# Optimization experiments

Hardware: AMD Instinct MI355X
Metric: run time of the kernel (lower is better)

## Reference

```python
import jax, jax.numpy as jnp
import numpy as np

V, NEIGH, C, N, H = 20000, 12, 16, 8, 4


def _circulant_basis(n):
    eye = jnp.eye(n, dtype=jnp.float32)
    return jnp.stack([jnp.roll(eye, b, axis=1) for b in range(n)])  # [n, n, n]


def setup_inputs() -> dict:
    key = jax.random.key(0)
    ks = jax.random.split(key, 12)
    x = jax.random.normal(ks[0], (V, C, N), dtype=jnp.float32)
    neighbors = jax.random.randint(ks[1], (V, NEIGH), 0, V)
    mask = jax.random.bernoulli(ks[2], 0.8, (V, NEIGH))
    pt = jax.random.normal(ks[3], (V, NEIGH, N, N), dtype=jnp.float32)
    rel_pos_u = jax.random.normal(ks[4], (V, NEIGH, 2), dtype=jnp.float32) * 0.1
    reg_basis = _circulant_basis(N)                                   # [N, N, N]
    value_basis1 = jax.random.normal(ks[5], (N, 2, N, N), dtype=jnp.float32)
    value_basis2 = jax.random.normal(ks[6], (N, 3, N, N), dtype=jnp.float32)
    s = 1.0 / np.sqrt(C * N)
    query_coeffs = jax.random.normal(ks[7], (H, C, N), dtype=jnp.float32) * s
    key_coeffs = jax.random.normal(ks[8], (H, C, N), dtype=jnp.float32) * s
    value0_params = jax.random.normal(ks[9], (H, C, N), dtype=jnp.float32) * s
    value1_params = jax.random.normal(ks[10], (H, C, N), dtype=jnp.float32) * s
    value2_params = jax.random.normal(ks[11], (H, C, N), dtype=jnp.float32) * s
    wm_weights = jax.random.normal(jax.random.fold_in(key, 99), (C, H * C, N), dtype=jnp.float32) * np.sqrt(2.0 / (H * C * N))
    return {"x": x, "neighbors": neighbors, "mask": mask,
            "parallel_transport_matrices": pt, "rel_pos_u": rel_pos_u,
            "reg_basis": reg_basis, "value_basis1": value_basis1,
            "value_basis2": value_basis2, "query_coeffs": query_coeffs,
            "key_coeffs": key_coeffs, "value0_params": value0_params,
            "value1_params": value1_params, "value2_params": value2_params,
            "wm_weights": wm_weights}


def reference(x, neighbors, mask, parallel_transport_matrices, rel_pos_u,
              reg_basis, value_basis1, value_basis2, query_coeffs, key_coeffs,
              value0_params, value1_params, value2_params, wm_weights):
    Nv, Cc, Nn = x.shape
    Hh = query_coeffs.shape[0]
    m = mask.astype(x.dtype)                                   # [v, n]
    x_neigh = x[neighbors] * m[:, :, None, None]               # [v, n, c, N]
    f = jnp.einsum('vnij,vncj->vnci', parallel_transport_matrices, x_neigh)
    # attention scores
    WQ = jnp.einsum('hcb,bij->hcij', query_coeffs, reg_basis)
    Q = jnp.einsum('hcij,vcj->vhi', WQ, x)                     # [v, h, N]
    WK = jnp.einsum('hcb,bij->hcij', key_coeffs, reg_basis)
    K = jnp.einsum('hcij,vncj->vnhi', WK, f)                   # [v, n, h, N]
    score = jax.nn.relu(Q[:, None] + K).mean(-1)               # [v, n, h]
    score = jnp.where(mask[:, :, None], score, 0.0)
    den = score.sum(axis=1)                                    # [v, h]
    dead = den < 1e-6
    n_valid = jnp.clip(m.sum(axis=1, keepdims=True), 1.0)      # [v, 1]
    uniform = m[:, :, None] / n_valid[:, :, None]              # [v, n, 1]
    attn = jnp.where(dead[:, None, :], uniform,
                     score / jnp.clip(den, 1e-6)[:, None, :])  # [v, n, h]
    # Taylor-basis values
    u0, u1 = rel_pos_u[..., 0], rel_pos_u[..., 1]
    u_quad = jnp.stack([u0 * u0, 2.0 * u0 * u1, u1 * u1], axis=-1)  # [v, n, 3]
    W0 = jnp.einsum('hcb,bij->hcij', value0_params, reg_basis)
    values = jnp.einsum('hcij,vncj->vnhci', W0, f)
    W1 = jnp.einsum('hcb,boij->hcoij', value1_params, value_basis1)
    values = values + jnp.einsum('hcoij,vncj,vno->vnhci', W1, f, rel_pos_u)
    W2 = jnp.einsum('hcb,boij->hcoij', value2_params, value_basis2)
    values = values + jnp.einsum('hcoij,vncj,vno->vnhci', W2, f, u_quad)
    head = jnp.einsum('vnh,vnhci->vhci', attn, values)         # [v, h, c, N]
    head = head.reshape(Nv, Hh * Cc, Nn)
    WM = jnp.einsum('ocb,bij->ocij', wm_weights, reg_basis)
    return jnp.einsum('ocij,vcj->voi', WM, head)               # [v, c, N]
```

## Files before the change

### kernel.cpp

```cpp
#include <hip/hip_runtime.h>

#define NV  20000
#define NNB 12
#define NC  16
#define NH  4
#define VC  4
#define GRID (NV/VC)

#define OFF_QC   0
#define OFF_KC   528
#define OFF_Q    1056
#define OFF_F    1184
#define OFF_HEAD 1184
#define OFF_SC   7520
#define OFF_DEN  7712
#define OFF_NV   7728
#define OFF_S4   7736
#define OFF_S2   7928
#define OFF_NB   8024
#define OFF_M    8072
#define SMEM_FL  8120

#define LD8(dst, off) { const float4 _a = *(const float4*)&smem[(off)]; \
                        const float4 _b = *(const float4*)&smem[(off)+4]; \
                        dst[0]=_a.x; dst[1]=_a.y; dst[2]=_a.z; dst[3]=_a.w; \
                        dst[4]=_b.x; dst[5]=_b.y; dst[6]=_b.z; dst[7]=_b.w; }
#define ST8(off, src) { *(float4*)&smem[(off)]   = make_float4(src[0],src[1],src[2],src[3]); \
                        *(float4*)&smem[(off)+4] = make_float4(src[4],src[5],src[6],src[7]); }

__global__ __launch_bounds__(256) void kprep(
    const float* __restrict__ v0p, const float* __restrict__ v1p,
    const float* __restrict__ v2p, const float* __restrict__ vb1,
    const float* __restrict__ vb2, float* __restrict__ A4,
    const unsigned char* __restrict__ m, int* __restrict__ flag)
{
    const int b = blockIdx.x, tid = threadIdx.x;
    if (b < 96) {
        int idx = b * 256 + tid;
        int j = idx & 7;
        int t = idx >> 3;
        int hc = t & 63; t >>= 6;
        int i = t & 7;
        int p = t >> 3;
        int h = hc >> 4, c = hc & 15;
        float s = 0.f;
        if (p == 0) {
            s = v0p[h*128 + c*8 + ((j - i + 8) & 7)];
        } else if (p <= 2) {
            int o = p - 1;
            #pragma unroll
            for (int bb = 0; bb < 8; ++bb)
                s += v1p[h*128 + c*8 + bb] * vb1[((bb*2 + o)*8 + i)*8 + j];
        } else {
            int o = p - 3;
            #pragma unroll
            for (int bb = 0; bb < 8; ++bb)
                s += v2p[h*128 + c*8 + bb] * vb2[((bb*3 + o)*8 + i)*8 + j];
        }
        A4[idx] = s;
    } else {
        __shared__ int s_nz;
        if (tid == 0) s_nz = 0;
        __syncthreads();
        int nz = 0;
        for (int k = (b - 96) * 256 + tid; k < NV * NNB; k += 64 * 256) {
            if ((k & 3) != 0 && m[k] != 0) nz = 1;
        }
        if (nz) atomicOr(&s_nz, 1);
        __syncthreads();
        if (tid == 0 && s_nz) atomicOr(flag, 1);
    }
}

__global__ __launch_bounds__(256, 4) void kmain(
    const float* __restrict__ x, const int* __restrict__ nbr,
    const unsigned char* __restrict__ mskb, const float* __restrict__ pt,
    const float* __restrict__ rel, const float* __restrict__ qc,
    const float* __restrict__ kc, const float* __restrict__ A4,
    const float* __restrict__ wm, const int* __restrict__ flagp,
    float* __restrict__ out)
{
    const int tid = threadIdx.x;
    const int vbase = blockIdx.x * VC;
    const int bytemode = flagp[0];
    const int* mski = (const int*)mskb;

    __shared__ __align__(16) float smem[SMEM_FL];

    for (int k = tid; k < 512; k += 256) {
        smem[OFF_QC + (k>>7)*132 + (k&127)] = qc[k];
        smem[OFF_KC + (k>>7)*132 + (k&127)] = kc[k];
    }
    if (tid < VC*NNB) {
        int gi = vbase*NNB + tid;
        ((int*)smem)[OFF_NB + tid] = nbr[gi];
        int raw = bytemode ? (int)mskb[gi] : mski[gi];
        smem[OFF_M + tid] = raw ? 1.0f : 0.0f;
    }
    if (tid >= 64 && tid < 64 + VC*NNB) {
        int vn = tid - 64;
        float u0 = rel[(vbase*NNB + vn)*2 + 0];
        float u1 = rel[(vbase*NNB + vn)*2 + 1];
        smem[OFF_S4+vn*4+0] = 1.0f;
        smem[OFF_S4+vn*4+1] = u0;
        smem[OFF_S4+vn*4+2] = u1;
        smem[OFF_S4+vn*4+3] = u0*u0;
        smem[OFF_S2+vn*2+0] = 2.0f*u0*u1;
        smem[OFF_S2+vn*2+1] = u1*u1;
    }
    __syncthreads();

    if (tid < 192) {
        const int vn = tid >> 2, cq = tid & 3;
        const int nb = ((const int*)smem)[OFF_NB + vn];
        const float m = smem[OFF_M + vn];
        const float4* xg = (const float4*)(x + (size_t)nb*128 + cq*32);
        float xnf[32];
        #pragma unroll
        for (int q = 0; q < 8; ++q) {
            float4 tv = xg[q];
            xnf[q*4+0]=tv.x; xnf[q*4+1]=tv.y; xnf[q*4+2]=tv.z; xnf[q*4+3]=tv.w;
        }
        const float* ptg = pt + (size_t)(vbase*NNB + vn)*64;
        float acc[4][8];
        #pragma unroll
        for (int c4 = 0; c4 < 4; ++c4)
            #pragma unroll
            for (int i = 0; i < 8; ++i) acc[c4][i] = 0.f;
        #pragma unroll
        for (int i = 0; i < 8; ++i) {
            const float4 pA = *(const float4*)(ptg + i*8);
            const float4 pB = *(const float4*)(ptg + i*8 + 4);
            float pj[8] = {pA.x,pA.y,pA.z,pA.w,pB.x,pB.y,pB.z,pB.w};
            #pragma unroll
            for (int c4 = 0; c4 < 4; ++c4)
                #pragma unroll
                for (int j = 0; j < 8; ++j)
                    acc[c4][i] += pj[j] * xnf[c4*8 + j];
        }
        #pragma unroll
        for (int c4 = 0; c4 < 4; ++c4) {
            int c = cq*4 + c4;
            float w[8];
            #pragma unroll
            for (int i = 0; i < 8; ++i) w[i] = m * acc[c4][i];
            ST8(OFF_F + vn*132 + c*8, w);
        }
    }
    __syncthreads();

    float K8[8] = {0,0,0,0,0,0,0,0};
    if (tid < 128) {
        const int cs = tid & 7, vh = tid >> 3, v = vh >> 2, h = vh & 3;
        const float* xrow = x + (size_t)(vbase + v)*128;
        float Q8[8] = {0,0,0,0,0,0,0,0};
        #pragma unroll
        for (int t = 0; t < 2; ++t) {
            int c = cs*2 + t;
            const float4 xa = *(const float4*)(xrow + c*8);
            const float4 xb = *(const float4*)(xrow + c*8 + 4);
            float xv[8] = {xa.x,xa.y,xa.z,xa.w,xb.x,xb.y,xb.z,xb.w};
            float qv[8]; LD8(qv, OFF_QC + h*132 + c*8);
            #pragma unroll
            for (int s = 0; s < 8; ++s)
                #pragma unroll
                for (int i = 0; i < 8; ++i)
                    Q8[i] += qv[s] * xv[(i+s)&7];
        }
        #pragma unroll
        for (int msk = 1; msk < 8; msk <<= 1)
            #pragma unroll
            for (int i = 0; i < 8; ++i) Q8[i] += __shfl_xor(Q8[i], msk, 64);
        if (cs == 0) { ST8(OFF_Q + vh*8, Q8); }
    }
    if (tid < 192) {
        const int vn = tid >> 2, h = tid & 3;
        #pragma unroll 2
        for (int c = 0; c < 16; ++c) {
            float kv[8]; LD8(kv, OFF_KC + h*132 + c*8);
            float fv[8]; LD8(fv, OFF_F + vn*132 + c*8);
            #pragma unroll
            for (int s = 0; s < 8; ++s)
                #pragma unroll
                for (int i = 0; i < 8; ++i)
                    K8[i] += kv[s] * fv[(i+s)&7];
        }
    }
    __syncthreads();

    if (tid < 192) {
        const int vn = tid >> 2, h = tid & 3, v = vn / 12;
        float q[8]; LD8(q, OFF_Q + (v*4+h)*8);
        float s = 0.f;
        #pragma unroll
        for (int i = 0; i < 8; ++i) s += fmaxf(0.f, q[i] + K8[i]);
        smem[OFF_SC + vn*4 + h] = 0.125f * s * smem[OFF_M + vn];
    }
    __syncthreads();

    if (tid < 16) {
        int v = tid >> 2, h = tid & 3;
        float d = 0.f;
        for (int n = 0; n < 12; ++n) d += smem[OFF_SC + (v*12+n)*4 + h];
        smem[OFF_DEN + tid] = d;
        if (h == 0) {
            float nv = 0.f;
            for (int n = 0; n < 12; ++n) nv += smem[OFF_M + v*12 + n];
            smem[OFF_NV + v] = fmaxf(nv, 1.0f);
        }
    }
    __syncthreads();
    if (tid < 192) {
        const int vn = tid >> 2, h = tid & 3, v = vn / 12;
        float den = smem[OFF_DEN + v*4 + h];
        float at = (den < 1e-6f) ? (smem[OFF_M + vn] / smem[OFF_NV + v])
                                 : (smem[OFF_SC + vn*4 + h] / fmaxf(den, 1e-6f));
        smem[OFF_SC + vn*4 + h] = at;
    }
    __syncthreads();

    const int v6 = tid >> 6, h6 = (tid >> 4) & 3, c6 = tid & 15, hc = tid & 63;
    float G[6][8];
    #pragma unroll
    for (int p = 0; p < 6; ++p)
        #pragma unroll
        for (int j = 0; j < 8; ++j) G[p][j] = 0.f;
    for (int n = 0; n < 12; ++n) {
        int vn = v6*12 + n;
        float at = smem[OFF_SC + vn*4 + h6];
        const float4 s4 = *(const float4*)&smem[OFF_S4 + vn*4];
        const float2 s2 = *(const float2*)&smem[OFF_S2 + vn*2];
        float fv[8]; LD8(fv, OFF_F + vn*132 + c6*8);
        float w[6] = {at*s4.x, at*s4.y, at*s4.z, at*s4.w, at*s2.x, at*s2.y};
        #pragma unroll
        for (int p = 0; p < 6; ++p)
            #pragma unroll
            for (int j = 0; j < 8; ++j) G[p][j] += w[p] * fv[j];
    }
    __syncthreads();

    float hd[8] = {0,0,0,0,0,0,0,0};
    #pragma unroll
    for (int p = 0; p < 6; ++p) {
        #pragma unroll
        for (int i = 0; i < 8; ++i) {
            const float4 a0 = *(const float4*)&A4[(((p*8+i)*64 + hc)*8)];
            const float4 a1 = *(const float4*)&A4[(((p*8+i)*64 + hc)*8) + 4];
            hd[i] += a0.x*G[p][0] + a0.y*G[p][1] + a0.z*G[p][2] + a0.w*G[p][3]
                   + a1.x*G[p][4] + a1.y*G[p][5] + a1.z*G[p][6] + a1.w*G[p][7];
        }
    }
    ST8(OFF_HEAD + v6*520 + hc*8, hd);
    __syncthreads();

    {
        const int v = tid >> 6, o = (tid >> 2) & 15, cs = tid & 3;
        float acc[8] = {0,0,0,0,0,0,0,0};
        #pragma unroll 2
        for (int cc = 0; cc < 16; ++cc) {
            int cp = cc*4 + cs;
            float hh[8]; LD8(hh, OFF_HEAD + v*520 + cp*8);
            const float4 w0 = *(const float4*)&wm[(o*64 + cp)*8];
            const float4 w1 = *(const float4*)&wm[(o*64 + cp)*8 + 4];
            float wv[8] = {w0.x,w0.y,w0.z,w0.w,w1.x,w1.y,w1.z,w1.w};
            #pragma unroll
            for (int d = 0; d < 8; ++d)
                #pragma unroll
                for (int i = 0; i < 8; ++i)
                    acc[i] += wv[d] * hh[(i+d)&7];
        }
        #pragma unroll
        for (int msk = 1; msk < 4; msk <<= 1)
            #pragma unroll
            for (int i = 0; i < 8; ++i) acc[i] += __shfl_xor(acc[i], msk, 64);
        if (cs == 0) {
            float* op = out + (size_t)(vbase + v)*128 + o*8;
            *(float4*)op       = make_float4(acc[0],acc[1],acc[2],acc[3]);
            *(float4*)(op + 4) = make_float4(acc[4],acc[5],acc[6],acc[7]);
        }
    }
}

extern "C" void kernel_launch(void* const* d_in, const int* in_sizes, int n_in,
                              void* d_out, int out_size, void* d_ws, size_t ws_size,
                              hipStream_t stream)
{
    const float* x   = (const float*)d_in[0];
    const int*   nbr = (const int*)d_in[1];
    const unsigned char* msk = (const unsigned char*)d_in[2];
    const float* pt  = (const float*)d_in[3];
    const float* rel = (const float*)d_in[4];
    const float* vb1 = (const float*)d_in[6];
    const float* vb2 = (const float*)d_in[7];
    const float* qc  = (const float*)d_in[8];
    const float* kc  = (const float*)d_in[9];
    const float* v0p = (const float*)d_in[10];
    const float* v1p = (const float*)d_in[11];
    const float* v2p = (const float*)d_in[12];
    const float* wm  = (const float*)d_in[13];

    int*   flag = (int*)d_ws;
    float* A4   = (float*)d_ws + 64;
    float* outp = (float*)d_out;

    hipMemsetAsync(d_ws, 0, 256, stream);
    hipLaunchKernelGGL(kprep, dim3(160),  dim3(256), 0, stream,
                       v0p, v1p, v2p, vb1, vb2, A4, msk, flag);
    hipLaunchKernelGGL(kmain, dim3(GRID), dim3(256), 0, stream,
                       x, nbr, msk, pt, rel, qc, kc, A4, wm, flag, outp);
}
```

Baseline: 268.8 us.

## Drop shared staging of coeffs/mask, overlap Q with transport, cut barriers

Removes the initial shared-memory staging of query/key coefficients, neighbor indices, masks and Taylor weights, reading them directly from global/L1 where needed. Query computation moves onto the otherwise idle threads 192-255, so it runs alongside the parallel-transport stage. The softmax denominator is computed redundantly per thread instead of in a separate 16-thread phase, which removes barriers. Shared memory shrinks and launch bounds rise to 6 waves for occupancy. The memset is dropped by having a single flag block write the flag directly with vectorized int4 mask scans. The cost is repeated global mask loads and extra register pressure.

```diff
diff --git a/kernel.cpp b/kernel.cpp
--- a/kernel.cpp
+++ b/kernel.cpp
@@ -2,24 +2,14 @@
 
 #define NV  20000
 #define NNB 12
-#define NC  16
-#define NH  4
 #define VC  4
 #define GRID (NV/VC)
 
-#define OFF_QC   0
-#define OFF_KC   528
-#define OFF_Q    1056
-#define OFF_F    1184
-#define OFF_HEAD 1184
-#define OFF_SC   7520
-#define OFF_DEN  7712
-#define OFF_NV   7728
-#define OFF_S4   7736
-#define OFF_S2   7928
-#define OFF_NB   8024
-#define OFF_M    8072
-#define SMEM_FL  8120
+#define OFF_Q    0
+#define OFF_F    128
+#define OFF_HEAD 128
+#define OFF_SC   6464
+#define SMEM_FL  6656
 
 #define LD8(dst, off) { const float4 _a = *(const float4*)&smem[(off)]; \
                         const float4 _b = *(const float4*)&smem[(off)+4]; \
@@ -62,17 +52,19 @@
         __shared__ int s_nz;
         if (tid == 0) s_nz = 0;
         __syncthreads();
+        const int4* mi4 = (const int4*)m;
         int nz = 0;
-        for (int k = (b - 96) * 256 + tid; k < NV * NNB; k += 64 * 256) {
-            if ((k & 3) != 0 && m[k] != 0) nz = 1;
+        for (int k = tid; k < (NV*NNB)/16; k += 256) {
+            int4 w = mi4[k];
+            nz |= (w.x | w.y | w.z | w.w) & 0xFFFFFF00;
         }
         if (nz) atomicOr(&s_nz, 1);
         __syncthreads();
-        if (tid == 0 && s_nz) atomicOr(flag, 1);
+        if (tid == 0) flag[0] = (s_nz != 0) ? 1 : 0;
     }
 }
 
-__global__ __launch_bounds__(256, 4) void kmain(
+__global__ __launch_bounds__(256, 6) void kmain(
     const float* __restrict__ x, const int* __restrict__ nbr,
     const unsigned char* __restrict__ mskb, const float* __restrict__ pt,
     const float* __restrict__ rel, const float* __restrict__ qc,
@@ -87,80 +79,48 @@
 
     __shared__ __align__(16) float smem[SMEM_FL];
 
-    for (int k = tid; k < 512; k += 256) {
-        smem[OFF_QC + (k>>7)*132 + (k&127)] = qc[k];
-        smem[OFF_KC + (k>>7)*132 + (k&127)] = kc[k];
-    }
-    if (tid < VC*NNB) {
-        int gi = vbase*NNB + tid;
-        ((int*)smem)[OFF_NB + tid] = nbr[gi];
-        int raw = bytemode ? (int)mskb[gi] : mski[gi];
-        smem[OFF_M + tid] = raw ? 1.0f : 0.0f;
-    }
-    if (tid >= 64 && tid < 64 + VC*NNB) {
-        int vn = tid - 64;
-        float u0 = rel[(vbase*NNB + vn)*2 + 0];
-        float u1 = rel[(vbase*NNB + vn)*2 + 1];
-        smem[OFF_S4+vn*4+0] = 1.0f;
-        smem[OFF_S4+vn*4+1] = u0;
-        smem[OFF_S4+vn*4+2] = u1;
-        smem[OFF_S4+vn*4+3] = u0*u0;
-        smem[OFF_S2+vn*2+0] = 2.0f*u0*u1;
-        smem[OFF_S2+vn*2+1] = u1*u1;
-    }
-    __syncthreads();
-
     if (tid < 192) {
         const int vn = tid >> 2, cq = tid & 3;
-        const int nb = ((const int*)smem)[OFF_NB + vn];
-        const float m = smem[OFF_M + vn];
+        const int gi = vbase*NNB + vn;
+        const int nb = nbr[gi];
+        const float m = (bytemode ? (int)mskb[gi] : mski[gi]) ? 1.0f : 0.0f;
         const float4* xg = (const float4*)(x + (size_t)nb*128 + cq*32);
-        float xnf[32];
-        #pragma unroll
-        for (int q = 0; q < 8; ++q) {
-            float4 tv = xg[q];
-            xnf[q*4+0]=tv.x; xnf[q*4+1]=tv.y; xnf[q*4+2]=tv.z; xnf[q*4+3]=tv.w;
-        }
-        const float* ptg = pt + (size_t)(vbase*NNB + vn)*64;
-        float acc[4][8];
-        #pragma unroll
-        for (int c4 = 0; c4 < 4; ++c4)
-            #pragma unroll
-            for (int i = 0; i < 8; ++i) acc[c4][i] = 0.f;
-        #pragma unroll
-        for (int i = 0; i < 8; ++i) {
-            const float4 pA = *(const float4*)(ptg + i*8);
-            const float4 pB = *(const float4*)(ptg + i*8 + 4);
-            float pj[8] = {pA.x,pA.y,pA.z,pA.w,pB.x,pB.y,pB.z,pB.w};
-            #pragma unroll
-            for (int c4 = 0; c4 < 4; ++c4)
-                #pragma unroll
-                for (int j = 0; j < 8; ++j)
-                    acc[c4][i] += pj[j] * xnf[c4*8 + j];
-        }
-        #pragma unroll
-        for (int c4 = 0; c4 < 4; ++c4) {
-            int c = cq*4 + c4;
-            float w[8];
-            #pragma unroll
-            for (int i = 0; i < 8; ++i) w[i] = m * acc[c4][i];
-            ST8(OFF_F + vn*132 + c*8, w);
-        }
-    }
-    __syncthreads();
-
-    float K8[8] = {0,0,0,0,0,0,0,0};
-    if (tid < 128) {
-        const int cs = tid & 7, vh = tid >> 3, v = vh >> 2, h = vh & 3;
+        const float* ptg = pt + (size_t)gi*64;
+        #pragma unroll
+        for (int cp2 = 0; cp2 < 2; ++cp2) {
+            const float4 xa0 = xg[cp2*4+0], xb0 = xg[cp2*4+1];
+            const float4 xa1 = xg[cp2*4+2], xb1 = xg[cp2*4+3];
+            float a0[8], a1[8];
+            #pragma unroll
+            for (int i = 0; i < 8; ++i) {
+                const float4 pA = *(const float4*)(ptg + i*8);
+                const float4 pB = *(const float4*)(ptg + i*8 + 4);
+                a0[i] = pA.x*xa0.x + pA.y*xa0.y + pA.z*xa0.z + pA.w*xa0.w
+                      + pB.x*xb0.x + pB.y*xb0.y + pB.z*xb0.z + pB.w*xb0.w;
+                a1[i] = pA.x*xa1.x + pA.y*xa1.y + pA.z*xa1.z + pA.w*xa1.w
+                      + pB.x*xb1.x + pB.y*xb1.y + pB.z*xb1.z + pB.w*xb1.w;
+            }
+            const int c0 = cq*4 + cp2*2;
+            float w0[8], w1[8];
+            #pragma unroll
+            for (int i = 0; i < 8; ++i) { w0[i] = m*a0[i]; w1[i] = m*a1[i]; }
+            ST8(OFF_F + vn*132 + c0*8, w0);
+            ST8(OFF_F + vn*132 + (c0+1)*8, w1);
+        }
+    } else {
+        const int t = tid - 192, v = t >> 4, h = (t >> 2) & 3, cs = t & 3;
         const float* xrow = x + (size_t)(vbase + v)*128;
+        const float* qcb  = qc + h*128;
         float Q8[8] = {0,0,0,0,0,0,0,0};
         #pragma unroll
-        for (int t = 0; t < 2; ++t) {
-            int c = cs*2 + t;
+        for (int q = 0; q < 4; ++q) {
+            const int c = cs*4 + q;
             const float4 xa = *(const float4*)(xrow + c*8);
             const float4 xb = *(const float4*)(xrow + c*8 + 4);
+            const float4 qa = *(const float4*)(qcb + c*8);
+            const float4 qb = *(const float4*)(qcb + c*8 + 4);
             float xv[8] = {xa.x,xa.y,xa.z,xa.w,xb.x,xb.y,xb.z,xb.w};
-            float qv[8]; LD8(qv, OFF_QC + h*132 + c*8);
+            float qv[8] = {qa.x,qa.y,qa.z,qa.w,qb.x,qb.y,qb.z,qb.w};
             #pragma unroll
             for (int s = 0; s < 8; ++s)
                 #pragma unroll
@@ -168,16 +128,23 @@
                     Q8[i] += qv[s] * xv[(i+s)&7];
         }
         #pragma unroll
-        for (int msk = 1; msk < 8; msk <<= 1)
-            #pragma unroll
-            for (int i = 0; i < 8; ++i) Q8[i] += __shfl_xor(Q8[i], msk, 64);
-        if (cs == 0) { ST8(OFF_Q + vh*8, Q8); }
-    }
+        for (int i = 0; i < 8; ++i) {
+            Q8[i] += __shfl_xor(Q8[i], 1, 64);
+            Q8[i] += __shfl_xor(Q8[i], 2, 64);
+        }
+        if (cs == 0) { ST8(OFF_Q + (v*4+h)*8, Q8); }
+    }
+    __syncthreads();
+
     if (tid < 192) {
-        const int vn = tid >> 2, h = tid & 3;
+        const int vn = tid >> 2, h = tid & 3, v = vn / 12;
+        const float* kcb = kc + h*128;
+        float K8[8] = {0,0,0,0,0,0,0,0};
         #pragma unroll 2
         for (int c = 0; c < 16; ++c) {
-            float kv[8]; LD8(kv, OFF_KC + h*132 + c*8);
+            const float4 ka = *(const float4*)(kcb + c*8);
+            const float4 kb = *(const float4*)(kcb + c*8 + 4);
+            float kv[8] = {ka.x,ka.y,ka.z,ka.w,kb.x,kb.y,kb.z,kb.w};
             float fv[8]; LD8(fv, OFF_F + vn*132 + c*8);
             #pragma unroll
             for (int s = 0; s < 8; ++s)
@@ -185,61 +152,61 @@
                 for (int i = 0; i < 8; ++i)
                     K8[i] += kv[s] * fv[(i+s)&7];
         }
-    }
-    __syncthreads();
-
+        float q8[8]; LD8(q8, OFF_Q + (v*4+h)*8);
+        const int gi = vbase*NNB + vn;
+        const float m = (bytemode ? (int)mskb[gi] : mski[gi]) ? 1.0f : 0.0f;
+        float s = 0.f;
+        #pragma unroll
+        for (int i = 0; i < 8; ++i) s += fmaxf(0.f, q8[i] + K8[i]);
+        smem[OFF_SC + vn*4 + h] = 0.125f * s * m;
+    }
+    __syncthreads();
+
+    float at = 0.f;
     if (tid < 192) {
-        const int vn = tid >> 2, h = tid & 3, v = vn / 12;
-        float q[8]; LD8(q, OFF_Q + (v*4+h)*8);
-        float s = 0.f;
-        #pragma unroll
-        for (int i = 0; i < 8; ++i) s += fmaxf(0.f, q[i] + K8[i]);
-        smem[OFF_SC + vn*4 + h] = 0.125f * s * smem[OFF_M + vn];
-    }
-    __syncthreads();
-
-    if (tid < 16) {
-        int v = tid >> 2, h = tid & 3;
-        float d = 0.f;
-        for (int n = 0; n < 12; ++n) d += smem[OFF_SC + (v*12+n)*4 + h];
-        smem[OFF_DEN + tid] = d;
-        if (h == 0) {
-            float nv = 0.f;
-            for (int n = 0; n < 12; ++n) nv += smem[OFF_M + v*12 + n];
-            smem[OFF_NV + v] = fmaxf(nv, 1.0f);
-        }
-    }
-    __syncthreads();
-    if (tid < 192) {
-        const int vn = tid >> 2, h = tid & 3, v = vn / 12;
-        float den = smem[OFF_DEN + v*4 + h];
-        float at = (den < 1e-6f) ? (smem[OFF_M + vn] / smem[OFF_NV + v])
-                                 : (smem[OFF_SC + vn*4 + h] / fmaxf(den, 1e-6f));
-        smem[OFF_SC + vn*4 + h] = at;
-    }
-    __syncthreads();
-
-    const int v6 = tid >> 6, h6 = (tid >> 4) & 3, c6 = tid & 15, hc = tid & 63;
+        const int vn = tid >> 2, h = tid & 3, v = vn / 12, nb0 = v*12;
+        float den = 0.f;
+        #pragma unroll
+        for (int n = 0; n < 12; ++n) den += smem[OFF_SC + (nb0+n)*4 + h];
+        float nv = 0.f;
+        #pragma unroll
+        for (int n = 0; n < 12; ++n) {
+            const int gi = vbase*NNB + nb0 + n;
+            nv += (bytemode ? (int)mskb[gi] : mski[gi]) ? 1.0f : 0.0f;
+        }
+        const int gi = vbase*NNB + vn;
+        const float m = (bytemode ? (int)mskb[gi] : mski[gi]) ? 1.0f : 0.0f;
+        const float sc = smem[OFF_SC + vn*4 + h];
+        at = (den < 1e-6f) ? (m / fmaxf(nv, 1.0f)) : (sc / fmaxf(den, 1e-6f));
+    }
+    __syncthreads();
+    if (tid < 192) smem[OFF_SC + (tid >> 2)*4 + (tid & 3)] = at;
+    __syncthreads();
+
+    const int v4 = tid >> 6, h4 = (tid >> 4) & 3, c4 = tid & 15, hc = tid & 63;
     float G[6][8];
     #pragma unroll
     for (int p = 0; p < 6; ++p)
         #pragma unroll
         for (int j = 0; j < 8; ++j) G[p][j] = 0.f;
+    const int gbase = vbase*NNB + v4*12;
     for (int n = 0; n < 12; ++n) {
-        int vn = v6*12 + n;
-        float at = smem[OFF_SC + vn*4 + h6];
-        const float4 s4 = *(const float4*)&smem[OFF_S4 + vn*4];
-        const float2 s2 = *(const float2*)&smem[OFF_S2 + vn*2];
-        float fv[8]; LD8(fv, OFF_F + vn*132 + c6*8);
-        float w[6] = {at*s4.x, at*s4.y, at*s4.z, at*s4.w, at*s2.x, at*s2.y};
+        const int vn = v4*12 + n;
+        const float a = smem[OFF_SC + vn*4 + h4];
+        const float2 uv = *(const float2*)(rel + (size_t)(gbase + n)*2);
+        float fv[8]; LD8(fv, OFF_F + vn*132 + c4*8);
+        const float w1 = a*uv.x, w2 = a*uv.y;
+        const float wv[6] = {a, w1, w2, w1*uv.x, 2.0f*w1*uv.y, w2*uv.y};
         #pragma unroll
         for (int p = 0; p < 6; ++p)
             #pragma unroll
-            for (int j = 0; j < 8; ++j) G[p][j] += w[p] * fv[j];
-    }
-    __syncthreads();
-
-    float hd[8] = {0,0,0,0,0,0,0,0};
+            for (int j = 0; j < 8; ++j) G[p][j] += wv[p] * fv[j];
+    }
+    __syncthreads();
+
+    float hd[8];
+    #pragma unroll
+    for (int i = 0; i < 8; ++i) hd[i] = 0.f;
     #pragma unroll
     for (int p = 0; p < 6; ++p) {
         #pragma unroll
@@ -250,7 +217,7 @@
                    + a1.x*G[p][4] + a1.y*G[p][5] + a1.z*G[p][6] + a1.w*G[p][7];
         }
     }
-    ST8(OFF_HEAD + v6*520 + hc*8, hd);
+    ST8(OFF_HEAD + v4*520 + hc*8, hd);
     __syncthreads();
 
     {
@@ -258,7 +225,7 @@
         float acc[8] = {0,0,0,0,0,0,0,0};
         #pragma unroll 2
         for (int cc = 0; cc < 16; ++cc) {
-            int cp = cc*4 + cs;
+            const int cp = cc*4 + cs;
             float hh[8]; LD8(hh, OFF_HEAD + v*520 + cp*8);
             const float4 w0 = *(const float4*)&wm[(o*64 + cp)*8];
             const float4 w1 = *(const float4*)&wm[(o*64 + cp)*8 + 4];
@@ -270,9 +237,10 @@
                     acc[i] += wv[d] * hh[(i+d)&7];
         }
         #pragma unroll
-        for (int msk = 1; msk < 4; msk <<= 1)
-            #pragma unroll
-            for (int i = 0; i < 8; ++i) acc[i] += __shfl_xor(acc[i], msk, 64);
+        for (int i = 0; i < 8; ++i) {
+            acc[i] += __shfl_xor(acc[i], 1, 64);
+            acc[i] += __shfl_xor(acc[i], 2, 64);
+        }
         if (cs == 0) {
             float* op = out + (size_t)(vbase + v)*128 + o*8;
             *(float4*)op       = make_float4(acc[0],acc[1],acc[2],acc[3]);
@@ -303,8 +271,7 @@
     float* A4   = (float*)d_ws + 64;
     float* outp = (float*)d_out;
 
-    hipMemsetAsync(d_ws, 0, 256, stream);
-    hipLaunchKernelGGL(kprep, dim3(160),  dim3(256), 0, stream,
+    hipLaunchKernelGGL(kprep, dim3(97),   dim3(256), 0, stream,
                        v0p, v1p, v2p, vb1, vb2, A4, msk, flag);
     hipLaunchKernelGGL(kmain, dim3(GRID), dim3(256), 0, stream,
                        x, nbr, msk, pt, rel, qc, kc, A4, wm, flag, outp);
```

New measurement: 410.8 us. 1.53x slower.
